# Optimization experiments

Measured on AMD Instinct MI355X. Metric: run time of the kernel, lower is better.

The kernel has to match this reference:

```python
import jax, jax.numpy as jnp
import numpy as np

EMBED_DIM = 512
N_HEADS = 8
HEAD_DIM = EMBED_DIM // N_HEADS
N_BINS = 512
MAX_BIN = 256
SCALE = 1.0 / np.sqrt(HEAD_DIM)


def _l2norm(x):
    # manifold.project onto unit sphere along last dim
    n = jnp.sqrt(jnp.sum(x * x, axis=-1, keepdims=True))
    return x / jnp.maximum(n, 1e-12)


def setup_inputs() -> dict:
    rng = jax.random.key(0)
    ks = jax.random.split(rng, 13)
    B, N, D = 1, 2048, EMBED_DIM
    s = 1.0 / np.sqrt(D)
    cen = jax.random.normal(ks[12], (N_BINS, HEAD_DIM), dtype=jnp.float32)
    return {
        "query": jax.random.normal(ks[0], (B, N, D), dtype=jnp.float32),
        "key": jax.random.normal(ks[1], (B, N, D), dtype=jnp.float32),
        "value": jax.random.normal(ks[2], (B, N, D), dtype=jnp.float32),
        "Wq": jax.random.normal(ks[3], (D, D), dtype=jnp.float32) * s,
        "bq": jax.random.normal(ks[4], (D,), dtype=jnp.float32) * s,
        "Wk": jax.random.normal(ks[5], (D, D), dtype=jnp.float32) * s,
        "bk": jax.random.normal(ks[6], (D,), dtype=jnp.float32) * s,
        "Wv": jax.random.normal(ks[7], (D, D), dtype=jnp.float32) * s,
        "bv": jax.random.normal(ks[8], (D,), dtype=jnp.float32) * s,
        "Wo": jax.random.normal(ks[9], (D, D), dtype=jnp.float32) * s,
        "bo": jax.random.normal(ks[10], (D,), dtype=jnp.float32) * s,
        "centroids": _l2norm(cen),  # unit bin centroids of dim head_dim
    }


def reference(query, key, value, Wq, bq, Wk, bk, Wv, bv, Wo, bo, centroids):
    B, Nq, D = query.shape
    Nk = key.shape[1]
    H, hd = N_HEADS, HEAD_DIM

    def split(x):  # [B,N,D] -> [B,H,N,hd]
        return x.reshape(B, -1, H, hd).transpose(0, 2, 1, 3)

    q = split(query @ Wq.T + bq)
    k = split(key @ Wk.T + bk)
    v = split(value @ Wv.T + bv)

    # manifold.project (sphere): attention uses the projected q/k, raw v
    qn = _l2norm(q)
    kn = _l2norm(k)

    # DavisCache: nearest-centroid bin id  [B,H,N]
    qb = jnp.argmax(jnp.einsum('bhnd,cd->bhnc', qn, centroids), axis=-1).astype(jnp.int32)
    kb = jnp.argmax(jnp.einsum('bhnd,cd->bhnc', kn, centroids), axis=-1).astype(jnp.int32)

    # neighboring_bins(qb, radius=1) on a ring: kb in {qb-1, qb, qb+1} mod N_BINS
    diff = (qb[..., :, None] - kb[..., None, :]) % N_BINS  # [B,H,Nq,Nk]
    neigh = (diff <= 1) | (diff >= N_BINS - 1)

    # truncate to first MAX_BIN selected keys (index order), as in the loop
    rank = jnp.cumsum(neigh.astype(jnp.int32), axis=-1)  # inclusive count
    sel = neigh & (rank <= MAX_BIN)
    # fallback: empty neighbor set -> all keys, then truncated to first MAX_BIN
    fallback = (jnp.arange(Nk, dtype=jnp.int32) < MAX_BIN)
    mask = jnp.where(neigh.any(axis=-1, keepdims=True), sel, fallback)

    scores = jnp.einsum('bhqd,bhkd->bhqk', qn, kn) * jnp.float32(SCALE)
    scores = jnp.where(mask, scores, jnp.float32(-1e30))
    attn = jax.nn.softmax(scores, axis=-1)  # dropout=0.0 (eval)
    out = jnp.einsum('bhqk,bhkd->bhqd', attn, v)

    out = out.transpose(0, 2, 1, 3).reshape(B, Nq, D)
    return out @ Wo.T + bo
```

## Files before the change

kernel.cpp:

```cpp
#include <hip/hip_runtime.h>
#include <hip/hip_bf16.h>

#define NTOK 2048
#define EMBED 512
#define NHEADS 8
#define HD 64
#define NBINS 512
#define MAXSEL 256

typedef unsigned short u16;
typedef unsigned int u32;

__device__ __forceinline__ float lof(u32 u){ return __uint_as_float(u << 16); }
__device__ __forceinline__ float hif(u32 u){ return __uint_as_float(u & 0xffff0000u); }
__device__ __forceinline__ float bf2f(u16 u){ return __uint_as_float(((u32)u) << 16); }
__device__ __forceinline__ u16 f2b(float f){
    __hip_bfloat16 h = __float2bfloat16(f);
    return *(u16*)&h;
}
__device__ __forceinline__ u32 pack2(float lo, float hi){
    return (u32)f2b(lo) | ((u32)f2b(hi) << 16);
}
__device__ __forceinline__ void fma8(const float* x, u32 ux, u32 uy, u32 uz, u32 uw, float& a){
    a += x[0]*lof(ux) + x[1]*hif(ux) + x[2]*lof(uy) + x[3]*hif(uy)
       + x[4]*lof(uz) + x[5]*hif(uz) + x[6]*lof(uw) + x[7]*hif(uw);
}

__device__ __forceinline__ u32 sniffp(const void* p){
    const u16* s = (const u16*)p;
    float m = 0.f;
    #pragma unroll
    for (int k=0; k<64; k++) m = fmaxf(m, fabsf(bf2f(s[2*k])));
    return (m > 100.f) ? 1u : 0u;
}

__global__ __launch_bounds__(256) void projqkv_kernel(
    const void* __restrict__ Xq, const void* __restrict__ Xk, const void* __restrict__ Xv,
    const void* __restrict__ Wq, const void* __restrict__ bq,
    const void* __restrict__ Wk, const void* __restrict__ bk,
    const void* __restrict__ Wv, const void* __restrict__ bv,
    const void* __restrict__ cen,
    void* __restrict__ outQ,
    u16* __restrict__ Kb, u16* __restrict__ Vb,
    u16* __restrict__ qbin, u16* __restrict__ kbin)
{
    int which = blockIdx.y;
    const void *X, *W, *Bb;
    if (which==0){ X=Xq; W=Wq; Bb=bq; }
    else if (which==1){ X=Xk; W=Wk; Bb=bk; }
    else { X=Xv; W=Wv; Bb=bv; }
    u32 fx = sniffp(X), fw = sniffp(W), fb = sniffp(Bb);
    int r0 = blockIdx.x * 8;
    int t = threadIdx.x;

    __shared__ __align__(16) float ubuf[4608];
    __shared__ __align__(16) float ps[64*65];
    __shared__ float nrm2[64][4];
    __shared__ float invn[64];
    __shared__ float bvl[64][8];
    __shared__ int   bil[64][8];

    float* xstage = ps;
    for (int i=t; i<1024; i+=256){
        int row = i>>7, c4 = i&127;
        float4 v;
        if (!fx){
            const u32* xp = (const u32*)((const u16*)X + (size_t)(r0+row)*EMBED);
            u32 a = xp[c4*2], b = xp[c4*2+1];
            v = make_float4(lof(a), hif(a), lof(b), hif(b));
        } else {
            v = ((const float4*)((const float*)X + (size_t)(r0+row)*EMBED))[c4];
        }
        *(float4*)(xstage + row*516 + c4*4) = v;
    }

    float acc2[8][2];
    #pragma unroll
    for (int r=0;r<8;r++){ acc2[r][0]=0.f; acc2[r][1]=0.f; }

    float4 pf[4];
    #pragma unroll
    for (int it=0; it<4; it++){
        int j = t + it*256, o = j>>1, half = j&1;
        if (!fw){
            const u32* wp2 = (const u32*)((const u16*)W + (size_t)o*EMBED + half*4);
            pf[it] = make_float4(lof(wp2[0]), hif(wp2[0]), lof(wp2[1]), hif(wp2[1]));
        } else {
            pf[it] = *(const float4*)((const float*)W + (size_t)o*EMBED + half*4);
        }
    }
    for (int k0=0; k0<512; k0+=8){
        __syncthreads();
        #pragma unroll
        for (int it=0; it<4; it++){
            int j = t + it*256, o = j>>1, kb = (j&1)*4;
            ubuf[o*9+kb+0]=pf[it].x; ubuf[o*9+kb+1]=pf[it].y;
            ubuf[o*9+kb+2]=pf[it].z; ubuf[o*9+kb+3]=pf[it].w;
        }
        if (k0+8 < 512){
            int kn = k0+8;
            #pragma unroll
            for (int it=0; it<4; it++){
                int j = t + it*256, o = j>>1, half = j&1;
                if (!fw){
                    const u32* wp2 = (const u32*)((const u16*)W + (size_t)o*EMBED + kn + half*4);
                    pf[it] = make_float4(lof(wp2[0]), hif(wp2[0]), lof(wp2[1]), hif(wp2[1]));
                } else {
                    pf[it] = *(const float4*)((const float*)W + (size_t)o*EMBED + kn + half*4);
                }
            }
        }
        __syncthreads();
        float w0[8], w1[8];
        #pragma unroll
        for (int kk=0;kk<8;kk++){
            w0[kk] = ubuf[t*9+kk];
            w1[kk] = ubuf[(t+256)*9+kk];
        }
        #pragma unroll
        for (int r=0;r<8;r++){
            const float* x = xstage + r*516 + k0;
            float4 x0 = *(const float4*)(x);
            float4 x1 = *(const float4*)(x+4);
            acc2[r][0] += x0.x*w0[0]+x0.y*w0[1]+x0.z*w0[2]+x0.w*w0[3]
                        + x1.x*w0[4]+x1.y*w0[5]+x1.z*w0[6]+x1.w*w0[7];
            acc2[r][1] += x0.x*w1[0]+x0.y*w1[1]+x0.z*w1[2]+x0.w*w1[3]
                        + x1.x*w1[4]+x1.y*w1[5]+x1.z*w1[6]+x1.w*w1[7];
        }
    }
    __syncthreads();
    {
        float b0 = fb ? ((const float*)Bb)[t]     : bf2f(((const u16*)Bb)[t]);
        float b1 = fb ? ((const float*)Bb)[t+256] : bf2f(((const u16*)Bb)[t+256]);
        int h0 = t>>6, c0 = t&63, h1 = (t+256)>>6, c1 = (t+256)&63;
        #pragma unroll
        for (int r=0;r<8;r++){
            ps[(r*8+h0)*65 + c0] = acc2[r][0]+b0;
            ps[(r*8+h1)*65 + c1] = acc2[r][1]+b1;
        }
    }
    __syncthreads();

    if (which == 2){
        int hr = t>>2, q4 = t&3;
        int row = hr>>3, head = hr&7;
        const float* src = ps + hr*65 + q4*16;
        u16* dst = Vb + (size_t)(r0+row)*EMBED + head*64 + q4*16;
        #pragma unroll
        for (int j8=0;j8<2;j8++){
            uint4 v;
            v.x = pack2(src[j8*8+0],src[j8*8+1]); v.y = pack2(src[j8*8+2],src[j8*8+3]);
            v.z = pack2(src[j8*8+4],src[j8*8+5]); v.w = pack2(src[j8*8+6],src[j8*8+7]);
            ((uint4*)dst)[j8] = v;
        }
        return;
    }

    u32 fc = sniffp(cen);
    int rg = t>>3, cg = t&7;
    float best[2] = {-3.4e38f,-3.4e38f};
    int   bidx[2] = {0,0};
    float cpre[16];
    #pragma unroll
    for (int it=0; it<16; it++){
        int e = t + it*256, j = e>>6, k = e&63;
        cpre[it] = fc ? ((const float*)cen)[(size_t)j*HD + k]
                      : bf2f(((const u16*)cen)[(size_t)j*HD + k]);
    }
    for (int tt=0; tt<8; tt++){
        __syncthreads();
        #pragma unroll
        for (int it=0; it<16; it++){
            int e = t + it*256, j = e>>6, k = e&63;
            ubuf[k*68 + j] = cpre[it];
        }
        if (tt < 7){
            #pragma unroll
            for (int it=0; it<16; it++){
                int e = t + it*256, j = e>>6, k = e&63;
                int gj = (tt+1)*64 + j;
                cpre[it] = fc ? ((const float*)cen)[(size_t)gj*HD + k]
                              : bf2f(((const u16*)cen)[(size_t)gj*HD + k]);
            }
        }
        __syncthreads();
        float acc[2][8];
        #pragma unroll
        for (int j=0;j<2;j++)
            #pragma unroll
            for (int c=0;c<8;c++) acc[j][c]=0.f;
        const float* pr0 = ps + (2*rg)*65;
        const float* pr1 = pr0 + 65;
        for (int k=0;k<64;k++){
            float a0 = pr0[k], a1 = pr1[k];
            const float4* cp = (const float4*)(ubuf + k*68 + cg*8);
            float4 c0 = cp[0], c1 = cp[1];
            acc[0][0]+=a0*c0.x; acc[0][1]+=a0*c0.y; acc[0][2]+=a0*c0.z; acc[0][3]+=a0*c0.w;
            acc[0][4]+=a0*c1.x; acc[0][5]+=a0*c1.y; acc[0][6]+=a0*c1.z; acc[0][7]+=a0*c1.w;
            acc[1][0]+=a1*c0.x; acc[1][1]+=a1*c0.y; acc[1][2]+=a1*c0.z; acc[1][3]+=a1*c0.w;
            acc[1][4]+=a1*c1.x; acc[1][5]+=a1*c1.y; acc[1][6]+=a1*c1.z; acc[1][7]+=a1*c1.w;
        }
        #pragma unroll
        for (int j=0;j<2;j++){
            #pragma unroll
            for (int c=0;c<8;c++){
                int gi = tt*64 + cg*8 + c;
                if (acc[j][c] > best[j]){ best[j]=acc[j][c]; bidx[j]=gi; }
            }
        }
    }
    bvl[2*rg  ][cg]=best[0]; bil[2*rg  ][cg]=bidx[0];
    bvl[2*rg+1][cg]=best[1]; bil[2*rg+1][cg]=bidx[1];
    {
        int hr = t>>2, q4 = t&3;
        const float* src = ps + hr*65 + q4*16;
        float ss=0.f;
        #pragma unroll
        for (int d=0;d<16;d++) ss += src[d]*src[d];
        nrm2[hr][q4]=ss;
    }
    __syncthreads();
    if (t < 64){
        int hr = t;
        invn[hr] = 1.f / fmaxf(sqrtf(nrm2[hr][0]+nrm2[hr][1]+nrm2[hr][2]+nrm2[hr][3]), 1e-12f);
        float bv = bvl[hr][0]; int bi = bil[hr][0];
        #pragma unroll
        for (int g=1; g<8; g++){
            float ov = bvl[hr][g]; int oi = bil[hr][g];
            if (ov > bv || (ov == bv && oi < bi)){ bv = ov; bi = oi; }
        }
        u16* bins = (which==0) ? qbin : kbin;
        int token = r0 + (hr>>3), head = hr&7;
        bins[head*NTOK + token] = (u16)bi;
    }
    __syncthreads();
    {
        int hr = t>>2, q4 = t&3;
        float inv = invn[hr];
        const float* src = ps + hr*65 + q4*16;
        int row = hr>>3, head = hr&7;
        size_t off = (size_t)(r0+row)*EMBED + head*64 + q4*16;
        if (which == 1){
            u16* dst = Kb + off;
            #pragma unroll
            for (int j8=0;j8<2;j8++){
                uint4 v;
                v.x = pack2(src[j8*8+0]*inv, src[j8*8+1]*inv);
                v.y = pack2(src[j8*8+2]*inv, src[j8*8+3]*inv);
                v.z = pack2(src[j8*8+4]*inv, src[j8*8+5]*inv);
                v.w = pack2(src[j8*8+6]*inv, src[j8*8+7]*inv);
                ((uint4*)dst)[j8] = v;
            }
        } else if (!fx){
            u16* dst = (u16*)outQ + off;
            #pragma unroll
            for (int j8=0;j8<2;j8++){
                uint4 v;
                v.x = pack2(src[j8*8+0]*inv, src[j8*8+1]*inv);
                v.y = pack2(src[j8*8+2]*inv, src[j8*8+3]*inv);
                v.z = pack2(src[j8*8+4]*inv, src[j8*8+5]*inv);
                v.w = pack2(src[j8*8+6]*inv, src[j8*8+7]*inv);
                ((uint4*)dst)[j8] = v;
            }
        } else {
            float* dst = (float*)outQ + off;
            #pragma unroll
            for (int j4=0;j4<4;j4++){
                float4 v = make_float4(src[j4*4+0]*inv, src[j4*4+1]*inv,
                                       src[j4*4+2]*inv, src[j4*4+3]*inv);
                ((float4*)dst)[j4] = v;
            }
        }
    }
}

__global__ __launch_bounds__(256) void attn_kernel(
    const void* __restrict__ query,
    const u16* __restrict__ Kb, const u16* __restrict__ Vb,
    const u16* __restrict__ qbin, const u16* __restrict__ kbin,
    void* __restrict__ out)
{
    u32 fq = sniffp(query);
    int q = blockIdx.x, t = threadIdx.x;
    int wave = t>>6, lane = t&63;
    __shared__ float qs[512];
    __shared__ float sc[4][256];
    __shared__ u16   sel[4][256];

    if (!fq){
        u32 u = ((const u32*)out)[(size_t)q*256 + t];
        qs[2*t] = lof(u); qs[2*t+1] = hif(u);
    } else {
        float2 f = ((const float2*)out)[(size_t)q*256 + t];
        qs[2*t] = f.x; qs[2*t+1] = f.y;
    }
    __syncthreads();

    for (int hh=0; hh<2; hh++){
        int h = wave*2 + hh;
        int myqb = qbin[h*NTOK + q];
        const uint4* kbp = (const uint4*)(kbin + h*NTOK + lane*32);
        u32 fl = 0;
        #pragma unroll
        for (int w4=0; w4<4; w4++){
            uint4 kw = kbp[w4];
            u32 arr[4] = {kw.x, kw.y, kw.z, kw.w};
            #pragma unroll
            for (int e=0;e<4;e++){
                int b0 = (int)(arr[e] & 0xffff), b1 = (int)(arr[e] >> 16);
                int d0 = (myqb - b0) & (NBINS-1), d1 = (myqb - b1) & (NBINS-1);
                if (d0 <= 1 || d0 >= NBINS-1) fl |= 1u << (w4*8 + e*2);
                if (d1 <= 1 || d1 >= NBINS-1) fl |= 1u << (w4*8 + e*2 + 1);
            }
        }
        int cnt = __popc(fl);
        int sum = cnt;
        #pragma unroll
        for (int off=1; off<64; off<<=1){
            int v = __shfl_up(sum, off, 64);
            if (lane >= off) sum += v;
        }
        int total = __shfl(sum, 63, 64);
        int r = sum - cnt;
        if (total){
            u32 f2 = fl;
            while (f2){
                int j = __ffs(f2) - 1; f2 &= f2 - 1;
                if (r < MAXSEL) sel[wave][r] = (u16)(lane*32 + j);
                r++;
            }
        } else {
            #pragma unroll
            for (int kq=0;kq<4;kq++) sel[wave][lane*4+kq] = (u16)(lane*4+kq);
        }
        int L = total ? min(total, MAXSEL) : MAXSEL;
        __syncthreads();
        const float* qh = qs + h*64;
        float mloc = -3.4e38f;
        for (int jj=lane; jj<L; jj+=64){
            int kkey = sel[wave][jj];
            const uint4* kr = (const uint4*)(Kb + (size_t)kkey*EMBED + h*64);
            float acc = 0.f;
            #pragma unroll
            for (int p=0;p<8;p++){ uint4 u = kr[p]; fma8(qh+p*8, u.x,u.y,u.z,u.w, acc); }
            float s = acc * 0.125f;
            sc[wave][jj] = s;
            mloc = fmaxf(mloc, s);
        }
        #pragma unroll
        for (int off=32; off; off>>=1) mloc = fmaxf(mloc, __shfl_xor(mloc, off, 64));
        float ssum = 0.f;
        for (int jj=lane; jj<L; jj+=64){
            float e = __expf(sc[wave][jj] - mloc);
            sc[wave][jj] = e; ssum += e;
        }
        #pragma unroll
        for (int off=32; off; off>>=1) ssum += __shfl_xor(ssum, off, 64);
        float inv = 1.f / fmaxf(ssum, 1e-37f);
        __syncthreads();
        float acc = 0.f;
        for (int j=0; j<L; j++){
            int kkey = sel[wave][j];
            acc += sc[wave][j] * bf2f(Vb[(size_t)kkey*EMBED + h*64 + lane]);
        }
        float o = acc * inv;
        if (!fq) ((u16*)out)[(size_t)q*EMBED + h*64 + lane] = f2b(o);
        else     ((float*)out)[(size_t)q*EMBED + h*64 + lane] = o;
        __syncthreads();
    }
}

__global__ __launch_bounds__(256) void oproj_kernel(
    void* __restrict__ out, const void* __restrict__ Wo, const void* __restrict__ bo)
{
    u32 fq = sniffp(out);
    u32 fw = sniffp(Wo), fb = sniffp(bo);
    int r0 = blockIdx.x * 4;
    int t = threadIdx.x;
    __shared__ __align__(16) float wsl[512*9];
    __shared__ __align__(16) float xst[4*516];

    for (int i=t; i<512; i+=256){
        int row = i>>7, c4 = i&127;
        float4 v;
        if (!fq){
            const u32* xp = (const u32*)((const u16*)out + (size_t)(r0+row)*EMBED);
            u32 a = xp[c4*2], b = xp[c4*2+1];
            v = make_float4(lof(a), hif(a), lof(b), hif(b));
        } else {
            v = ((const float4*)((const float*)out + (size_t)(r0+row)*EMBED))[c4];
        }
        *(float4*)(xst + row*516 + c4*4) = v;
    }

    float acc2[4][2];
    #pragma unroll
    for (int r=0;r<4;r++){ acc2[r][0]=0.f; acc2[r][1]=0.f; }

    float4 pf[4];
    #pragma unroll
    for (int it=0; it<4; it++){
        int j = t + it*256, o = j>>1, half = j&1;
        if (!fw){
            const u32* wp2 = (const u32*)((const u16*)Wo + (size_t)o*EMBED + half*4);
            pf[it] = make_float4(lof(wp2[0]), hif(wp2[0]), lof(wp2[1]), hif(wp2[1]));
        } else {
            pf[it] = *(const float4*)((const float*)Wo + (size_t)o*EMBED + half*4);
        }
    }
    for (int k0=0; k0<512; k0+=8){
        __syncthreads();
        #pragma unroll
        for (int it=0; it<4; it++){
            int j = t + it*256, o = j>>1, kb = (j&1)*4;
            wsl[o*9+kb+0]=pf[it].x; wsl[o*9+kb+1]=pf[it].y;
            wsl[o*9+kb+2]=pf[it].z; wsl[o*9+kb+3]=pf[it].w;
        }
        if (k0+8 < 512){
            int kn = k0+8;
            #pragma unroll
            for (int it=0; it<4; it++){
                int j = t + it*256, o = j>>1, half = j&1;
                if (!fw){
                    const u32* wp2 = (const u32*)((const u16*)Wo + (size_t)o*EMBED + kn + half*4);
                    pf[it] = make_float4(lof(wp2[0]), hif(wp2[0]), lof(wp2[1]), hif(wp2[1]));
                } else {
                    pf[it] = *(const float4*)((const float*)Wo + (size_t)o*EMBED + kn + half*4);
                }
            }
        }
        __syncthreads();
        float w0[8], w1[8];
        #pragma unroll
        for (int kk=0;kk<8;kk++){
            w0[kk] = wsl[t*9+kk];
            w1[kk] = wsl[(t+256)*9+kk];
        }
        #pragma unroll
        for (int r=0;r<4;r++){
            const float* x = xst + r*516 + k0;
            float4 x0 = *(const float4*)(x);
            float4 x1 = *(const float4*)(x+4);
            acc2[r][0] += x0.x*w0[0]+x0.y*w0[1]+x0.z*w0[2]+x0.w*w0[3]
                        + x1.x*w0[4]+x1.y*w0[5]+x1.z*w0[6]+x1.w*w0[7];
            acc2[r][1] += x0.x*w1[0]+x0.y*w1[1]+x0.z*w1[2]+x0.w*w1[3]
                        + x1.x*w1[4]+x1.y*w1[5]+x1.z*w1[6]+x1.w*w1[7];
        }
    }
    float b0 = fb ? ((const float*)bo)[t]     : bf2f(((const u16*)bo)[t]);
    float b1 = fb ? ((const float*)bo)[t+256] : bf2f(((const u16*)bo)[t+256]);
    if (!fq){
        u16* o = (u16*)out;
        #pragma unroll
        for (int r=0;r<4;r++){
            o[(size_t)(r0+r)*EMBED + t]       = f2b(acc2[r][0]+b0);
            o[(size_t)(r0+r)*EMBED + t + 256] = f2b(acc2[r][1]+b1);
        }
    } else {
        float* o = (float*)out;
        #pragma unroll
        for (int r=0;r<4;r++){
            o[(size_t)(r0+r)*EMBED + t]       = acc2[r][0]+b0;
            o[(size_t)(r0+r)*EMBED + t + 256] = acc2[r][1]+b1;
        }
    }
}

extern "C" void kernel_launch(void* const* d_in, const int* in_sizes, int n_in,
                              void* d_out, int out_size, void* d_ws, size_t ws_size,
                              hipStream_t stream)
{
    const void* query = d_in[0];
    const void* key   = d_in[1];
    const void* value = d_in[2];
    const void* Wq = d_in[3];
    const void* bq = d_in[4];
    const void* Wk = d_in[5];
    const void* bk = d_in[6];
    const void* Wv = d_in[7];
    const void* bv = d_in[8];
    const void* Wo = d_in[9];
    const void* bo = d_in[10];
    const void* cen = d_in[11];

    char* ws = (char*)d_ws;
    u16* qbin = (u16*)ws;
    u16* kbin = (u16*)(ws + 32768);
    u16* Kb   = (u16*)(ws + 65536);
    u16* Vb   = (u16*)(ws + 65536 + (size_t)2*1024*1024);

    projqkv_kernel<<<dim3(256,3), 256, 0, stream>>>(query,key,value,Wq,bq,Wk,bk,Wv,bv,cen,
                                                    d_out,Kb,Vb,qbin,kbin);
    attn_kernel<<<2048, 256, 0, stream>>>(query,Kb,Vb,qbin,kbin,d_out);
    oproj_kernel<<<512, 256, 0, stream>>>(d_out,Wo,bo);
}
```

Before: 319.1 us.

## Move V and output projections to bf16 MFMA and parallelize heads in attention

Splits the V projection out of the fused QKV kernel into a dedicated kernel that uses bf16 MFMA 16x16x32 instructions, and rewrites the output projection the same way in place of the scalar FMA loop. The attention kernel now runs 512 threads, one wave per head, so all eight heads proceed concurrently without block-wide barriers between them. Weights are read directly from global memory per MFMA tile without shared-memory staging, and fp32 inputs get rounded to bf16, which lowers precision on the fp32 path.

```diff
diff --git a/kernel.cpp b/kernel.cpp
--- a/kernel.cpp
+++ b/kernel.cpp
@@ -10,6 +10,8 @@
 
 typedef unsigned short u16;
 typedef unsigned int u32;
+typedef short s16x8 __attribute__((ext_vector_type(8)));
+typedef float f32x4 __attribute__((ext_vector_type(4)));
 
 __device__ __forceinline__ float lof(u32 u){ return __uint_as_float(u << 16); }
 __device__ __forceinline__ float hif(u32 u){ return __uint_as_float(u & 0xffff0000u); }
@@ -34,21 +36,19 @@
     return (m > 100.f) ? 1u : 0u;
 }
 
-__global__ __launch_bounds__(256) void projqkv_kernel(
-    const void* __restrict__ Xq, const void* __restrict__ Xk, const void* __restrict__ Xv,
+__global__ __launch_bounds__(256) void projqk_kernel(
+    const void* __restrict__ Xq, const void* __restrict__ Xk,
     const void* __restrict__ Wq, const void* __restrict__ bq,
     const void* __restrict__ Wk, const void* __restrict__ bk,
-    const void* __restrict__ Wv, const void* __restrict__ bv,
     const void* __restrict__ cen,
     void* __restrict__ outQ,
-    u16* __restrict__ Kb, u16* __restrict__ Vb,
+    u16* __restrict__ Kb,
     u16* __restrict__ qbin, u16* __restrict__ kbin)
 {
     int which = blockIdx.y;
-    const void *X, *W, *Bb;
-    if (which==0){ X=Xq; W=Wq; Bb=bq; }
-    else if (which==1){ X=Xk; W=Wk; Bb=bk; }
-    else { X=Xv; W=Wv; Bb=bv; }
+    const void *X = which ? Xk : Xq;
+    const void *W = which ? Wk : Wq;
+    const void *Bb = which ? bk : bq;
     u32 fx = sniffp(X), fw = sniffp(W), fb = sniffp(Bb);
     int r0 = blockIdx.x * 8;
     int t = threadIdx.x;
@@ -140,21 +140,6 @@
         }
     }
     __syncthreads();
-
-    if (which == 2){
-        int hr = t>>2, q4 = t&3;
-        int row = hr>>3, head = hr&7;
-        const float* src = ps + hr*65 + q4*16;
-        u16* dst = Vb + (size_t)(r0+row)*EMBED + head*64 + q4*16;
-        #pragma unroll
-        for (int j8=0;j8<2;j8++){
-            uint4 v;
-            v.x = pack2(src[j8*8+0],src[j8*8+1]); v.y = pack2(src[j8*8+2],src[j8*8+3]);
-            v.z = pack2(src[j8*8+4],src[j8*8+5]); v.w = pack2(src[j8*8+6],src[j8*8+7]);
-            ((uint4*)dst)[j8] = v;
-        }
-        return;
-    }
 
     u32 fc = sniffp(cen);
     int rg = t>>3, cg = t&7;
@@ -274,100 +259,160 @@
     }
 }
 
-__global__ __launch_bounds__(256) void attn_kernel(
+__global__ __launch_bounds__(256) void projv_kernel(
+    const void* __restrict__ Xv, const void* __restrict__ Wv, const void* __restrict__ bv,
+    u16* __restrict__ Vb)
+{
+    u32 fx = sniffp(Xv), fw = sniffp(Wv), fb = sniffp(bv);
+    int r0 = blockIdx.x * 16;
+    int t = threadIdx.x;
+    __shared__ u16 xsb[16*520];
+
+    {
+        int row = t>>4, seg = t&15;
+        u16* dst = xsb + row*520 + seg*32;
+        if (!fx){
+            const uint4* src = (const uint4*)((const u16*)Xv + (size_t)(r0+row)*EMBED + seg*32);
+            #pragma unroll
+            for (int j=0;j<4;j++) ((uint4*)dst)[j] = src[j];
+        } else {
+            const float4* src = (const float4*)((const float*)Xv + (size_t)(r0+row)*EMBED + seg*32);
+            #pragma unroll
+            for (int j=0;j<4;j++){
+                float4 a = src[j*2], b = src[j*2+1];
+                uint4 v;
+                v.x = pack2(a.x,a.y); v.y = pack2(a.z,a.w);
+                v.z = pack2(b.x,b.y); v.w = pack2(b.z,b.w);
+                ((uint4*)dst)[j] = v;
+            }
+        }
+    }
+    __syncthreads();
+    int lane = t&63, wave = t>>6;
+    int m = lane&15, quad = lane>>4;
+    int obase = wave*128;
+    f32x4 acc[8];
+    #pragma unroll
+    for (int i=0;i<8;i++){ f32x4 z = {0.f,0.f,0.f,0.f}; acc[i] = z; }
+    const u16* arow = xsb + m*520 + quad*8;
+    for (int k=0;k<16;k++){
+        s16x8 a = *(const s16x8*)(arow + k*32);
+        #pragma unroll
+        for (int tile=0;tile<8;tile++){
+            int o = obase + tile*16 + m;
+            s16x8 b;
+            if (!fw){
+                b = *(const s16x8*)((const u16*)Wv + (size_t)o*EMBED + k*32 + quad*8);
+            } else {
+                const float4* wp = (const float4*)((const float*)Wv + (size_t)o*EMBED + k*32 + quad*8);
+                float4 w0 = wp[0], w1 = wp[1];
+                union { u32 u[4]; s16x8 v; } bb;
+                bb.u[0] = pack2(w0.x,w0.y); bb.u[1] = pack2(w0.z,w0.w);
+                bb.u[2] = pack2(w1.x,w1.y); bb.u[3] = pack2(w1.z,w1.w);
+                b = bb.v;
+            }
+            acc[tile] = __builtin_amdgcn_mfma_f32_16x16x32_bf16(a, b, acc[tile], 0, 0, 0);
+        }
+    }
+    #pragma unroll
+    for (int tile=0;tile<8;tile++){
+        int o = obase + tile*16 + m;
+        float bias = fb ? ((const float*)bv)[o] : bf2f(((const u16*)bv)[o]);
+        #pragma unroll
+        for (int reg=0;reg<4;reg++){
+            int row = quad*4 + reg;
+            Vb[(size_t)(r0+row)*EMBED + o] = f2b(acc[tile][reg] + bias);
+        }
+    }
+}
+
+__global__ __launch_bounds__(512) void attn_kernel(
     const void* __restrict__ query,
     const u16* __restrict__ Kb, const u16* __restrict__ Vb,
     const u16* __restrict__ qbin, const u16* __restrict__ kbin,
     void* __restrict__ out)
 {
     u32 fq = sniffp(query);
-    int q = blockIdx.x, t = threadIdx.x;
-    int wave = t>>6, lane = t&63;
-    __shared__ float qs[512];
-    __shared__ float sc[4][256];
-    __shared__ u16   sel[4][256];
-
-    if (!fq){
-        u32 u = ((const u32*)out)[(size_t)q*256 + t];
-        qs[2*t] = lof(u); qs[2*t+1] = hif(u);
+    int q = blockIdx.x;
+    int h = threadIdx.x >> 6;
+    int lane = threadIdx.x & 63;
+    __shared__ float qsh[8][64];
+    __shared__ float sc[8][256];
+    __shared__ u16   sel[8][256];
+
+    {
+        float qv;
+        if (!fq) qv = bf2f(((const u16*)out)[(size_t)q*EMBED + h*64 + lane]);
+        else     qv = ((const float*)out)[(size_t)q*EMBED + h*64 + lane];
+        qsh[h][lane] = qv;
+    }
+    int myqb = qbin[h*NTOK + q];
+    const uint4* kbp = (const uint4*)(kbin + h*NTOK + lane*32);
+    u32 fl = 0;
+    #pragma unroll
+    for (int w4=0; w4<4; w4++){
+        uint4 kw = kbp[w4];
+        u32 arr[4] = {kw.x, kw.y, kw.z, kw.w};
+        #pragma unroll
+        for (int e=0;e<4;e++){
+            int b0 = (int)(arr[e] & 0xffff), b1 = (int)(arr[e] >> 16);
+            int d0 = (myqb - b0) & (NBINS-1), d1 = (myqb - b1) & (NBINS-1);
+            if (d0 <= 1 || d0 >= NBINS-1) fl |= 1u << (w4*8 + e*2);
+            if (d1 <= 1 || d1 >= NBINS-1) fl |= 1u << (w4*8 + e*2 + 1);
+        }
+    }
+    int cnt = __popc(fl);
+    int sum = cnt;
+    #pragma unroll
+    for (int off=1; off<64; off<<=1){
+        int v = __shfl_up(sum, off, 64);
+        if (lane >= off) sum += v;
+    }
+    int total = __shfl(sum, 63, 64);
+    int r = sum - cnt;
+    if (total){
+        u32 f2 = fl;
+        while (f2){
+            int j = __ffs(f2) - 1; f2 &= f2 - 1;
+            if (r < MAXSEL) sel[h][r] = (u16)(lane*32 + j);
+            r++;
+        }
     } else {
-        float2 f = ((const float2*)out)[(size_t)q*256 + t];
-        qs[2*t] = f.x; qs[2*t+1] = f.y;
-    }
-    __syncthreads();
-
-    for (int hh=0; hh<2; hh++){
-        int h = wave*2 + hh;
-        int myqb = qbin[h*NTOK + q];
-        const uint4* kbp = (const uint4*)(kbin + h*NTOK + lane*32);
-        u32 fl = 0;
-        #pragma unroll
-        for (int w4=0; w4<4; w4++){
-            uint4 kw = kbp[w4];
-            u32 arr[4] = {kw.x, kw.y, kw.z, kw.w};
-            #pragma unroll
-            for (int e=0;e<4;e++){
-                int b0 = (int)(arr[e] & 0xffff), b1 = (int)(arr[e] >> 16);
-                int d0 = (myqb - b0) & (NBINS-1), d1 = (myqb - b1) & (NBINS-1);
-                if (d0 <= 1 || d0 >= NBINS-1) fl |= 1u << (w4*8 + e*2);
-                if (d1 <= 1 || d1 >= NBINS-1) fl |= 1u << (w4*8 + e*2 + 1);
-            }
-        }
-        int cnt = __popc(fl);
-        int sum = cnt;
-        #pragma unroll
-        for (int off=1; off<64; off<<=1){
-            int v = __shfl_up(sum, off, 64);
-            if (lane >= off) sum += v;
-        }
-        int total = __shfl(sum, 63, 64);
-        int r = sum - cnt;
-        if (total){
-            u32 f2 = fl;
-            while (f2){
-                int j = __ffs(f2) - 1; f2 &= f2 - 1;
-                if (r < MAXSEL) sel[wave][r] = (u16)(lane*32 + j);
-                r++;
-            }
-        } else {
-            #pragma unroll
-            for (int kq=0;kq<4;kq++) sel[wave][lane*4+kq] = (u16)(lane*4+kq);
-        }
-        int L = total ? min(total, MAXSEL) : MAXSEL;
-        __syncthreads();
-        const float* qh = qs + h*64;
-        float mloc = -3.4e38f;
-        for (int jj=lane; jj<L; jj+=64){
-            int kkey = sel[wave][jj];
-            const uint4* kr = (const uint4*)(Kb + (size_t)kkey*EMBED + h*64);
-            float acc = 0.f;
-            #pragma unroll
-            for (int p=0;p<8;p++){ uint4 u = kr[p]; fma8(qh+p*8, u.x,u.y,u.z,u.w, acc); }
-            float s = acc * 0.125f;
-            sc[wave][jj] = s;
-            mloc = fmaxf(mloc, s);
-        }
-        #pragma unroll
-        for (int off=32; off; off>>=1) mloc = fmaxf(mloc, __shfl_xor(mloc, off, 64));
-        float ssum = 0.f;
-        for (int jj=lane; jj<L; jj+=64){
-            float e = __expf(sc[wave][jj] - mloc);
-            sc[wave][jj] = e; ssum += e;
-        }
-        #pragma unroll
-        for (int off=32; off; off>>=1) ssum += __shfl_xor(ssum, off, 64);
-        float inv = 1.f / fmaxf(ssum, 1e-37f);
-        __syncthreads();
+        #pragma unroll
+        for (int kq=0;kq<4;kq++) sel[h][lane*4+kq] = (u16)(lane*4+kq);
+    }
+    int L = total ? min(total, MAXSEL) : MAXSEL;
+
+    const float* qh = qsh[h];
+    float mloc = -3.4e38f;
+    for (int jj=lane; jj<L; jj+=64){
+        int kkey = sel[h][jj];
+        const uint4* kr = (const uint4*)(Kb + (size_t)kkey*EMBED + h*64);
         float acc = 0.f;
-        for (int j=0; j<L; j++){
-            int kkey = sel[wave][j];
-            acc += sc[wave][j] * bf2f(Vb[(size_t)kkey*EMBED + h*64 + lane]);
-        }
-        float o = acc * inv;
-        if (!fq) ((u16*)out)[(size_t)q*EMBED + h*64 + lane] = f2b(o);
-        else     ((float*)out)[(size_t)q*EMBED + h*64 + lane] = o;
-        __syncthreads();
-    }
+        #pragma unroll
+        for (int p=0;p<8;p++){ uint4 u = kr[p]; fma8(qh+p*8, u.x,u.y,u.z,u.w, acc); }
+        float s = acc * 0.125f;
+        sc[h][jj] = s;
+        mloc = fmaxf(mloc, s);
+    }
+    #pragma unroll
+    for (int off=32; off; off>>=1) mloc = fmaxf(mloc, __shfl_xor(mloc, off, 64));
+    float ssum = 0.f;
+    for (int jj=lane; jj<L; jj+=64){
+        float e = __expf(sc[h][jj] - mloc);
+        sc[h][jj] = e; ssum += e;
+    }
+    #pragma unroll
+    for (int off=32; off; off>>=1) ssum += __shfl_xor(ssum, off, 64);
+    float inv = 1.f / fmaxf(ssum, 1e-37f);
+    float acc = 0.f;
+    for (int j=0; j<L; j++){
+        int kkey = sel[h][j];
+        acc += sc[h][j] * bf2f(Vb[(size_t)kkey*EMBED + h*64 + lane]);
+    }
+    float o = acc * inv;
+    if (!fq) ((u16*)out)[(size_t)q*EMBED + h*64 + lane] = f2b(o);
+    else     ((float*)out)[(size_t)q*EMBED + h*64 + lane] = o;
 }
 
 __global__ __launch_bounds__(256) void oproj_kernel(
@@ -375,93 +420,66 @@
 {
     u32 fq = sniffp(out);
     u32 fw = sniffp(Wo), fb = sniffp(bo);
-    int r0 = blockIdx.x * 4;
+    int r0 = blockIdx.x * 16;
     int t = threadIdx.x;
-    __shared__ __align__(16) float wsl[512*9];
-    __shared__ __align__(16) float xst[4*516];
-
-    for (int i=t; i<512; i+=256){
-        int row = i>>7, c4 = i&127;
-        float4 v;
+    __shared__ u16 ab[16*520];
+
+    {
+        int row = t>>4, seg = t&15;
+        u16* dst = ab + row*520 + seg*32;
         if (!fq){
-            const u32* xp = (const u32*)((const u16*)out + (size_t)(r0+row)*EMBED);
-            u32 a = xp[c4*2], b = xp[c4*2+1];
-            v = make_float4(lof(a), hif(a), lof(b), hif(b));
+            const uint4* src = (const uint4*)((const u16*)out + (size_t)(r0+row)*EMBED + seg*32);
+            #pragma unroll
+            for (int j=0;j<4;j++) ((uint4*)dst)[j] = src[j];
         } else {
-            v = ((const float4*)((const float*)out + (size_t)(r0+row)*EMBED))[c4];
-        }
-        *(float4*)(xst + row*516 + c4*4) = v;
-    }
-
-    float acc2[4][2];
-    #pragma unroll
-    for (int r=0;r<4;r++){ acc2[r][0]=0.f; acc2[r][1]=0.f; }
-
-    float4 pf[4];
-    #pragma unroll
-    for (int it=0; it<4; it++){
-        int j = t + it*256, o = j>>1, half = j&1;
-        if (!fw){
-            const u32* wp2 = (const u32*)((const u16*)Wo + (size_t)o*EMBED + half*4);
-            pf[it] = make_float4(lof(wp2[0]), hif(wp2[0]), lof(wp2[1]), hif(wp2[1]));
-        } else {
-            pf[it] = *(const float4*)((const float*)Wo + (size_t)o*EMBED + half*4);
-        }
-    }
-    for (int k0=0; k0<512; k0+=8){
-        __syncthreads();
-        #pragma unroll
-        for (int it=0; it<4; it++){
-            int j = t + it*256, o = j>>1, kb = (j&1)*4;
-            wsl[o*9+kb+0]=pf[it].x; wsl[o*9+kb+1]=pf[it].y;
-            wsl[o*9+kb+2]=pf[it].z; wsl[o*9+kb+3]=pf[it].w;
-        }
-        if (k0+8 < 512){
-            int kn = k0+8;
-            #pragma unroll
-            for (int it=0; it<4; it++){
-                int j = t + it*256, o = j>>1, half = j&1;
-                if (!fw){
-                    const u32* wp2 = (const u32*)((const u16*)Wo + (size_t)o*EMBED + kn + half*4);
-                    pf[it] = make_float4(lof(wp2[0]), hif(wp2[0]), lof(wp2[1]), hif(wp2[1]));
-                } else {
-                    pf[it] = *(const float4*)((const float*)Wo + (size_t)o*EMBED + kn + half*4);
-                }
-            }
-        }
-        __syncthreads();
-        float w0[8], w1[8];
-        #pragma unroll
-        for (int kk=0;kk<8;kk++){
-            w0[kk] = wsl[t*9+kk];
-            w1[kk] = wsl[(t+256)*9+kk];
-        }
-        #pragma unroll
-        for (int r=0;r<4;r++){
-            const float* x = xst + r*516 + k0;
-            float4 x0 = *(const float4*)(x);
-            float4 x1 = *(const float4*)(x+4);
-            acc2[r][0] += x0.x*w0[0]+x0.y*w0[1]+x0.z*w0[2]+x0.w*w0[3]
-                        + x1.x*w0[4]+x1.y*w0[5]+x1.z*w0[6]+x1.w*w0[7];
-            acc2[r][1] += x0.x*w1[0]+x0.y*w1[1]+x0.z*w1[2]+x0.w*w1[3]
-                        + x1.x*w1[4]+x1.y*w1[5]+x1.z*w1[6]+x1.w*w1[7];
-        }
-    }
-    float b0 = fb ? ((const float*)bo)[t]     : bf2f(((const u16*)bo)[t]);
-    float b1 = fb ? ((const float*)bo)[t+256] : bf2f(((const u16*)bo)[t+256]);
-    if (!fq){
-        u16* o = (u16*)out;
-        #pragma unroll
-        for (int r=0;r<4;r++){
-            o[(size_t)(r0+r)*EMBED + t]       = f2b(acc2[r][0]+b0);
-            o[(size_t)(r0+r)*EMBED + t + 256] = f2b(acc2[r][1]+b1);
-        }
-    } else {
-        float* o = (float*)out;
-        #pragma unroll
-        for (int r=0;r<4;r++){
-            o[(size_t)(r0+r)*EMBED + t]       = acc2[r][0]+b0;
-            o[(size_t)(r0+r)*EMBED + t + 256] = acc2[r][1]+b1;
+            const float4* src = (const float4*)((const float*)out + (size_t)(r0+row)*EMBED + seg*32);
+            #pragma unroll
+            for (int j=0;j<4;j++){
+                float4 a = src[j*2], b = src[j*2+1];
+                uint4 v;
+                v.x = pack2(a.x,a.y); v.y = pack2(a.z,a.w);
+                v.z = pack2(b.x,b.y); v.w = pack2(b.z,b.w);
+                ((uint4*)dst)[j] = v;
+            }
+        }
+    }
+    __syncthreads();
+    int lane = t&63, wave = t>>6;
+    int m = lane&15, quad = lane>>4;
+    int obase = wave*128;
+    f32x4 acc[8];
+    #pragma unroll
+    for (int i=0;i<8;i++){ f32x4 z = {0.f,0.f,0.f,0.f}; acc[i] = z; }
+    const u16* arow = ab + m*520 + quad*8;
+    for (int k=0;k<16;k++){
+        s16x8 a = *(const s16x8*)(arow + k*32);
+        #pragma unroll
+        for (int tile=0;tile<8;tile++){
+            int o = obase + tile*16 + m;
+            s16x8 b;
+            if (!fw){
+                b = *(const s16x8*)((const u16*)Wo + (size_t)o*EMBED + k*32 + quad*8);
+            } else {
+                const float4* wp = (const float4*)((const float*)Wo + (size_t)o*EMBED + k*32 + quad*8);
+                float4 w0 = wp[0], w1 = wp[1];
+                union { u32 u[4]; s16x8 v; } bb;
+                bb.u[0] = pack2(w0.x,w0.y); bb.u[1] = pack2(w0.z,w0.w);
+                bb.u[2] = pack2(w1.x,w1.y); bb.u[3] = pack2(w1.z,w1.w);
+                b = bb.v;
+            }
+            acc[tile] = __builtin_amdgcn_mfma_f32_16x16x32_bf16(a, b, acc[tile], 0, 0, 0);
+        }
+    }
+    #pragma unroll
+    for (int tile=0;tile<8;tile++){
+        int o = obase + tile*16 + m;
+        float bias = fb ? ((const float*)bo)[o] : bf2f(((const u16*)bo)[o]);
+        #pragma unroll
+        for (int reg=0;reg<4;reg++){
+            int row = quad*4 + reg;
+            float v = acc[tile][reg] + bias;
+            if (!fq) ((u16*)out)[(size_t)(r0+row)*EMBED + o] = f2b(v);
+            else     ((float*)out)[(size_t)(r0+row)*EMBED + o] = v;
         }
     }
 }
@@ -489,8 +507,9 @@
     u16* Kb   = (u16*)(ws + 65536);
     u16* Vb   = (u16*)(ws + 65536 + (size_t)2*1024*1024);
 
-    projqkv_kernel<<<dim3(256,3), 256, 0, stream>>>(query,key,value,Wq,bq,Wk,bk,Wv,bv,cen,
-                                                    d_out,Kb,Vb,qbin,kbin);
-    attn_kernel<<<2048, 256, 0, stream>>>(query,Kb,Vb,qbin,kbin,d_out);
-    oproj_kernel<<<512, 256, 0, stream>>>(d_out,Wo,bo);
-}
+    projqk_kernel<<<dim3(256,2), 256, 0, stream>>>(query,key,Wq,bq,Wk,bk,cen,
+                                                   d_out,Kb,qbin,kbin);
+    projv_kernel<<<128, 256, 0, stream>>>(value,Wv,bv,Vb);
+    attn_kernel<<<2048, 512, 0, stream>>>(query,Kb,Vb,qbin,kbin,d_out);
+    oproj_kernel<<<128, 256, 0, stream>>>(d_out,Wo,bo);
+}
```

New measurement: 343.1 us. +7.5%, slower.
